# Performance work log

Measured on AMD Instinct MI355X. Metric: run time of the kernel, lower is better.

The kernel has to match this reference:

```python
import jax, jax.numpy as jnp
import numpy as np


def setup_inputs() -> dict:
    key = jax.random.key(0)
    k1, k2, k3 = jax.random.split(key, 3)
    B, C_in, H, W = 16, 256, 64, 64
    C_out, KH, KW = 256, 3, 3
    x = jax.random.normal(k1, (B, C_in, H, W), dtype=jnp.float32)
    # kaiming-uniform-like scale for realism
    fan_in = C_in * KH * KW
    bound = 1.0 / np.sqrt(fan_in)
    weights = jax.random.normal(k2, (C_out, C_in, KH, KW), dtype=jnp.float32) * bound
    bias = jax.random.uniform(k3, (C_out,), dtype=jnp.float32, minval=-bound, maxval=bound)
    return {"x": x, "weights": weights, "bias": bias}


def reference(x, weights, bias):
    # Conv2dApproximation with approximation_enable=False is an exact conv2d:
    # input is unfolded to [B, C*kh*kw, oh, ow], weights to [C_out, C*kh*kw],
    # and the MultiApp kernel performs the exact MAC (see exact matmul backward).
    # stride=(1,1), padding=(0,0), dilation=(1,1) per init_kwargs.
    out = jax.lax.conv_general_dilated(
        x, weights,
        window_strides=(1, 1),
        padding=((0, 0), (0, 0)),
        rhs_dilation=(1, 1),
        dimension_numbers=("NCHW", "OIHW", "NCHW"),
    )
    return out + bias[None, :, None, None]
```

## Files before the change

### kernel.cpp

```cpp
#include <hip/hip_runtime.h>
#include <stdint.h>

typedef short short8 __attribute__((ext_vector_type(8)));
typedef float f32x4 __attribute__((ext_vector_type(4)));

#define AS1 __attribute__((address_space(1)))
#define AS3 __attribute__((address_space(3)))

__device__ __forceinline__ void gl_lds16(const void* g, void* l) {
  __builtin_amdgcn_global_load_lds((const AS1 unsigned int*)g,
                                   (AS3 unsigned int*)l, 16, 0, 0);
}

__device__ __forceinline__ unsigned short f2bf(float f) {
  union { float f; unsigned int u; } v; v.f = f;
  return (unsigned short)((v.u + (((v.u >> 16) & 1u) + 0x7fffu)) >> 16);
}

__global__ __launch_bounds__(256) void xpose_kernel(const float* __restrict__ x,
                                                    unsigned short* __restrict__ xt) {
  __shared__ float tile[64][68];
  const int bid = blockIdx.x;
  const int cchunk = bid & 3;
  const int y = (bid >> 2) & 63;
  const int b = bid >> 8;
  const int t = threadIdx.x;
  const int ci0 = cchunk * 64;

  const int cc = t >> 2;
  const int xo = (t & 3) * 16;
  const float* src = x + (((size_t)(b * 256 + ci0 + cc) * 64 + y) * 64 + xo);
  float4 v0 = ((const float4*)src)[0];
  float4 v1 = ((const float4*)src)[1];
  float4 v2 = ((const float4*)src)[2];
  float4 v3 = ((const float4*)src)[3];
  *(float4*)&tile[cc][xo + 0]  = v0;
  *(float4*)&tile[cc][xo + 4]  = v1;
  *(float4*)&tile[cc][xo + 8]  = v2;
  *(float4*)&tile[cc][xo + 12] = v3;
  __syncthreads();

  const int xpos = t >> 2;
  const int ccg = (t & 3) * 16;
  unsigned int pk[8];
#pragma unroll
  for (int e = 0; e < 8; ++e) {
    unsigned int lo = f2bf(tile[ccg + 2 * e][xpos]);
    unsigned int hi = f2bf(tile[ccg + 2 * e + 1][xpos]);
    pk[e] = lo | (hi << 16);
  }
  unsigned short* dst = xt + ((size_t)(b * 4096 + y * 64 + xpos) * 256 + ci0 + ccg);
  uint4 w0; w0.x = pk[0]; w0.y = pk[1]; w0.z = pk[2]; w0.w = pk[3];
  uint4 w1; w1.x = pk[4]; w1.y = pk[5]; w1.z = pk[6]; w1.w = pk[7];
  ((uint4*)dst)[0] = w0;
  ((uint4*)dst)[1] = w1;
}

__global__ __launch_bounds__(256) void wpack_kernel(const float* __restrict__ w,
                                                    unsigned short* __restrict__ wrp) {
  const int idx = blockIdx.x * 256 + threadIdx.x;
  const int ci = idx & 255;
  const int co = (idx >> 8) & 255;
  const int p = idx >> 16;
  wrp[idx] = f2bf(w[(size_t)(co * 256 + ci) * 9 + p]);
}

__global__ __launch_bounds__(512, 2) void conv_mfma8(
    const unsigned short* __restrict__ xt,
    const unsigned short* __restrict__ wrp,
    const float* __restrict__ bias,
    float* __restrict__ out) {
  __shared__ unsigned short lds[4 * 16384];

  const int tid = threadIdx.x;
  const int lane = tid & 63;
  const int wv = tid >> 6;
  const int wr = wv >> 2;
  const int wc = wv & 3;
  const int bid = blockIdx.x;
  const int b = bid >> 4;
  const int oh0 = (bid & 15) * 4;

  const int srow = tid >> 2;
  const int sslot = tid & 3;
  const int sl = sslot ^ ((srow >> 1) & 3);
  const unsigned short* gA0 = wrp + (size_t)srow * 256 + sl * 8;
  const unsigned short* gA1 = wrp + (size_t)(128 + srow) * 256 + sl * 8;
  const unsigned short* gB[2];
#pragma unroll
  for (int i = 0; i < 2; ++i) {
    const int px = i * 128 + srow;
    const int prow = px >> 6, pcol = px & 63;
    const int y = min(oh0 + prow, 61);
    const int xc = min(pcol, 61);
    gB[i] = xt + ((size_t)(b * 64 + y) * 64 + xc) * 256 + sl * 8;
  }
  const unsigned ldsA0 = wv * 512;
  const unsigned ldsA1 = 4096 + wv * 512;
  const unsigned ldsB0 = 8192 + wv * 512;
  const unsigned ldsB1 = 12288 + wv * 512;

  int aoff[4], boff[8];
#pragma unroll
  for (int m = 0; m < 4; ++m) {
    const int row = wc * 64 + m * 16 + (lane & 15);
    const int s = (lane >> 4) ^ ((row >> 1) & 3);
    aoff[m] = row * 32 + s * 8;
  }
#pragma unroll
  for (int n = 0; n < 8; ++n) {
    const int row = wr * 128 + n * 16 + (lane & 15);
    const int s = (lane >> 4) ^ ((row >> 1) & 3);
    boff[n] = 8192 + row * 32 + s * 8;
  }

  auto stageA = [&](int kt) {
    const int tap = kt >> 3, chunk = (kt & 7) * 32;
    const int Aoff = tap * 65536 + chunk;
    unsigned short* base = lds + (kt & 3) * 16384;
    gl_lds16(gA0 + Aoff, base + ldsA0);
    gl_lds16(gA1 + Aoff, base + ldsA1);
  };
  auto stageB = [&](int kt) {
    const int tap = kt >> 3, chunk = (kt & 7) * 32;
    const int kh = (tap * 11) >> 5, kw = tap - kh * 3;
    const int Boff = (kh * 64 + kw) * 256 + chunk;
    unsigned short* base = lds + (kt & 3) * 16384;
    gl_lds16(gB[0] + Boff, base + ldsB0);
    gl_lds16(gB[1] + Boff, base + ldsB1);
  };

  f32x4 acc[4][8] = {};

  stageA(0); stageB(0);
  stageA(1); stageB(1);
  stageA(2); stageB(2);
  asm volatile("s_waitcnt vmcnt(8)" ::: "memory");
  __builtin_amdgcn_s_barrier();

  for (int kt = 0; kt < 72; ++kt) {
    unsigned short* buf = lds + (kt & 3) * 16384;
    short8 a[4], bq[4];
#pragma unroll
    for (int m = 0; m < 4; ++m) a[m] = *(const short8*)(buf + aoff[m]);
#pragma unroll
    for (int n = 0; n < 4; ++n) bq[n] = *(const short8*)(buf + boff[n]);
    if (kt < 69) stageA(kt + 3);
    __builtin_amdgcn_s_barrier();
    asm volatile("s_waitcnt lgkmcnt(0)" ::: "memory");
    __builtin_amdgcn_sched_barrier(0);
    __builtin_amdgcn_s_setprio(1);
#pragma unroll
    for (int m = 0; m < 4; ++m)
#pragma unroll
      for (int n = 0; n < 4; ++n)
        acc[m][n] = __builtin_amdgcn_mfma_f32_16x16x32_bf16(a[m], bq[n], acc[m][n], 0, 0, 0);
    __builtin_amdgcn_s_setprio(0);
    __builtin_amdgcn_s_barrier();
#pragma unroll
    for (int n = 0; n < 4; ++n) bq[n] = *(const short8*)(buf + boff[4 + n]);
    if (kt < 69) stageB(kt + 3);
    __builtin_amdgcn_s_barrier();
    asm volatile("s_waitcnt lgkmcnt(0)" ::: "memory");
    __builtin_amdgcn_sched_barrier(0);
    __builtin_amdgcn_s_setprio(1);
#pragma unroll
    for (int m = 0; m < 4; ++m)
#pragma unroll
      for (int n = 0; n < 4; ++n)
        acc[m][4 + n] = __builtin_amdgcn_mfma_f32_16x16x32_bf16(a[m], bq[n], acc[m][4 + n], 0, 0, 0);
    __builtin_amdgcn_s_setprio(0);
    if (kt <= 68)      asm volatile("s_waitcnt vmcnt(8)" ::: "memory");
    else if (kt == 69) asm volatile("s_waitcnt vmcnt(4)" ::: "memory");
    else if (kt == 70) asm volatile("s_waitcnt vmcnt(0)" ::: "memory");
    __builtin_amdgcn_s_barrier();
  }

  const int rb = (lane >> 4) * 4;
  const int colp = lane & 15;
  float bv[4][4];
#pragma unroll
  for (int m = 0; m < 4; ++m)
#pragma unroll
    for (int j = 0; j < 4; ++j)
      bv[m][j] = bias[wc * 64 + m * 16 + rb + j];
#pragma unroll
  for (int m = 0; m < 4; ++m) {
#pragma unroll
    for (int n = 0; n < 8; ++n) {
      const int px = wr * 128 + n * 16 + colp;
      const int prow = px >> 6, ow = px & 63;
      const int oh = oh0 + prow;
      if (ow < 62 && oh < 62) {
#pragma unroll
        for (int j = 0; j < 4; ++j) {
          const int co = wc * 64 + m * 16 + rb + j;
          out[((size_t)(b * 256 + co) * 62 + oh) * 62 + ow] = acc[m][n][j] + bv[m][j];
        }
      }
    }
  }
}

__global__ __launch_bounds__(256) void conv_naive(const float* __restrict__ x,
                                                  const float* __restrict__ wgt,
                                                  const float* __restrict__ bias,
                                                  float* __restrict__ out) {
  const size_t idx = (size_t)blockIdx.x * 256 + threadIdx.x;
  if (idx >= (size_t)16 * 256 * 62 * 62) return;
  const int ow = (int)(idx % 62);
  size_t r = idx / 62;
  const int oh = (int)(r % 62); r /= 62;
  const int co = (int)(r % 256);
  const int b = (int)(r / 256);
  float s = bias[co];
  for (int ci = 0; ci < 256; ++ci) {
    const float* xp = x + ((size_t)(b * 256 + ci) * 64 + oh) * 64 + ow;
    const float* wp = wgt + (size_t)(co * 256 + ci) * 9;
#pragma unroll
    for (int kh = 0; kh < 3; ++kh)
#pragma unroll
      for (int kw = 0; kw < 3; ++kw)
        s += xp[kh * 64 + kw] * wp[kh * 3 + kw];
  }
  out[idx] = s;
}

extern "C" void kernel_launch(void* const* d_in, const int* in_sizes, int n_in,
                              void* d_out, int out_size, void* d_ws, size_t ws_size,
                              hipStream_t stream) {
  const float* x = (const float*)d_in[0];
  const float* wgt = (const float*)d_in[1];
  const float* bias = (const float*)d_in[2];
  float* out = (float*)d_out;

  const size_t xt_elems = (size_t)16 * 64 * 64 * 256;
  const size_t wr_elems = (size_t)9 * 256 * 256;
  const size_t need = (xt_elems + wr_elems) * sizeof(unsigned short);

  if (ws_size < need) {
    conv_naive<<<61504, 256, 0, stream>>>(x, wgt, bias, out);
    return;
  }

  unsigned short* xt = (unsigned short*)d_ws;
  unsigned short* wrp = xt + xt_elems;

  xpose_kernel<<<4096, 256, 0, stream>>>(x, xt);
  wpack_kernel<<<2304, 256, 0, stream>>>(wgt, wrp);
  conv_mfma8<<<256, 512, 0, stream>>>(xt, wrp, bias, out);
}
```

Baseline: 101.2 us.

## Split output channels across blocks, shrink tiles and use 3-stage pipeline

```diff
diff --git a/kernel.cpp b/kernel.cpp
--- a/kernel.cpp
+++ b/kernel.cpp
@@ -65,42 +65,43 @@
   wrp[idx] = f2bf(w[(size_t)(co * 256 + ci) * 9 + p]);
 }
 
-__global__ __launch_bounds__(512, 2) void conv_mfma8(
+__global__ __launch_bounds__(512, 4) void conv_mfma2(
     const unsigned short* __restrict__ xt,
     const unsigned short* __restrict__ wrp,
     const float* __restrict__ bias,
     float* __restrict__ out) {
-  __shared__ unsigned short lds[4 * 16384];
+  __shared__ unsigned short lds[3 * 12288];
 
   const int tid = threadIdx.x;
   const int lane = tid & 63;
   const int wv = tid >> 6;
-  const int wr = wv >> 2;
-  const int wc = wv & 3;
+  const int wc = wv & 1;
+  const int wp = wv >> 1;
   const int bid = blockIdx.x;
-  const int b = bid >> 4;
+  const int cohalf = bid >> 8;
+  const int b = (bid >> 4) & 15;
   const int oh0 = (bid & 15) * 4;
-
-  const int srow = tid >> 2;
-  const int sslot = tid & 3;
-  const int sl = sslot ^ ((srow >> 1) & 3);
-  const unsigned short* gA0 = wrp + (size_t)srow * 256 + sl * 8;
-  const unsigned short* gA1 = wrp + (size_t)(128 + srow) * 256 + sl * 8;
+  const int co0 = cohalf * 128;
+
+  const int l2 = lane >> 2;
+  const int l3 = lane & 3;
+  const int rA = wv * 16 + l2;
+  const int slA = l3 ^ ((rA >> 1) & 3);
+  const unsigned short* gA = wrp + (size_t)(co0 + rA) * 256 + slA * 8;
   const unsigned short* gB[2];
 #pragma unroll
   for (int i = 0; i < 2; ++i) {
-    const int px = i * 128 + srow;
-    const int prow = px >> 6, pcol = px & 63;
-    const int y = min(oh0 + prow, 61);
-    const int xc = min(pcol, 61);
+    const int r = wv * 32 + i * 16 + l2;
+    const int sl = l3 ^ ((r >> 1) & 3);
+    const int y = min(oh0 + (r >> 6), 61);
+    const int xc = min(r & 63, 61);
     gB[i] = xt + ((size_t)(b * 64 + y) * 64 + xc) * 256 + sl * 8;
   }
-  const unsigned ldsA0 = wv * 512;
-  const unsigned ldsA1 = 4096 + wv * 512;
-  const unsigned ldsB0 = 8192 + wv * 512;
-  const unsigned ldsB1 = 12288 + wv * 512;
-
-  int aoff[4], boff[8];
+  const unsigned ldsA  = wv * 512;
+  const unsigned ldsB0 = 4096 + wv * 1024;
+  const unsigned ldsB1 = 4096 + wv * 1024 + 512;
+
+  int aoff[4], boff[4];
 #pragma unroll
   for (int m = 0; m < 4; ++m) {
     const int row = wc * 64 + m * 16 + (lane & 15);
@@ -108,45 +109,37 @@
     aoff[m] = row * 32 + s * 8;
   }
 #pragma unroll
-  for (int n = 0; n < 8; ++n) {
-    const int row = wr * 128 + n * 16 + (lane & 15);
+  for (int n = 0; n < 4; ++n) {
+    const int row = wp * 64 + n * 16 + (lane & 15);
     const int s = (lane >> 4) ^ ((row >> 1) & 3);
-    boff[n] = 8192 + row * 32 + s * 8;
-  }
-
-  auto stageA = [&](int kt) {
-    const int tap = kt >> 3, chunk = (kt & 7) * 32;
-    const int Aoff = tap * 65536 + chunk;
-    unsigned short* base = lds + (kt & 3) * 16384;
-    gl_lds16(gA0 + Aoff, base + ldsA0);
-    gl_lds16(gA1 + Aoff, base + ldsA1);
-  };
-  auto stageB = [&](int kt) {
+    boff[n] = 4096 + row * 32 + s * 8;
+  }
+
+  auto stage = [&](int kt) {
     const int tap = kt >> 3, chunk = (kt & 7) * 32;
     const int kh = (tap * 11) >> 5, kw = tap - kh * 3;
+    unsigned short* base = lds + (kt % 3) * 12288;
+    gl_lds16(gA + tap * 65536 + chunk, base + ldsA);
     const int Boff = (kh * 64 + kw) * 256 + chunk;
-    unsigned short* base = lds + (kt & 3) * 16384;
     gl_lds16(gB[0] + Boff, base + ldsB0);
     gl_lds16(gB[1] + Boff, base + ldsB1);
   };
 
-  f32x4 acc[4][8] = {};
-
-  stageA(0); stageB(0);
-  stageA(1); stageB(1);
-  stageA(2); stageB(2);
-  asm volatile("s_waitcnt vmcnt(8)" ::: "memory");
+  f32x4 acc[4][4] = {};
+
+  stage(0);
+  stage(1);
+  asm volatile("s_waitcnt vmcnt(3)" ::: "memory");
   __builtin_amdgcn_s_barrier();
 
   for (int kt = 0; kt < 72; ++kt) {
-    unsigned short* buf = lds + (kt & 3) * 16384;
-    short8 a[4], bq[4];
+    unsigned short* buf = lds + (kt % 3) * 12288;
+    short8 a[4], bb[4];
 #pragma unroll
     for (int m = 0; m < 4; ++m) a[m] = *(const short8*)(buf + aoff[m]);
 #pragma unroll
-    for (int n = 0; n < 4; ++n) bq[n] = *(const short8*)(buf + boff[n]);
-    if (kt < 69) stageA(kt + 3);
-    __builtin_amdgcn_s_barrier();
+    for (int n = 0; n < 4; ++n) bb[n] = *(const short8*)(buf + boff[n]);
+    if (kt < 70) stage(kt + 2);
     asm volatile("s_waitcnt lgkmcnt(0)" ::: "memory");
     __builtin_amdgcn_sched_barrier(0);
     __builtin_amdgcn_s_setprio(1);
@@ -154,49 +147,30 @@
     for (int m = 0; m < 4; ++m)
 #pragma unroll
       for (int n = 0; n < 4; ++n)
-        acc[m][n] = __builtin_amdgcn_mfma_f32_16x16x32_bf16(a[m], bq[n], acc[m][n], 0, 0, 0);
+        acc[m][n] = __builtin_amdgcn_mfma_f32_16x16x32_bf16(a[m], bb[n], acc[m][n], 0, 0, 0);
     __builtin_amdgcn_s_setprio(0);
-    __builtin_amdgcn_s_barrier();
-#pragma unroll
-    for (int n = 0; n < 4; ++n) bq[n] = *(const short8*)(buf + boff[4 + n]);
-    if (kt < 69) stageB(kt + 3);
-    __builtin_amdgcn_s_barrier();
-    asm volatile("s_waitcnt lgkmcnt(0)" ::: "memory");
-    __builtin_amdgcn_sched_barrier(0);
-    __builtin_amdgcn_s_setprio(1);
-#pragma unroll
-    for (int m = 0; m < 4; ++m)
-#pragma unroll
-      for (int n = 0; n < 4; ++n)
-        acc[m][4 + n] = __builtin_amdgcn_mfma_f32_16x16x32_bf16(a[m], bq[n], acc[m][4 + n], 0, 0, 0);
-    __builtin_amdgcn_s_setprio(0);
-    if (kt <= 68)      asm volatile("s_waitcnt vmcnt(8)" ::: "memory");
-    else if (kt == 69) asm volatile("s_waitcnt vmcnt(4)" ::: "memory");
+    if (kt < 70)       asm volatile("s_waitcnt vmcnt(3)" ::: "memory");
     else if (kt == 70) asm volatile("s_waitcnt vmcnt(0)" ::: "memory");
     __builtin_amdgcn_s_barrier();
   }
 
   const int rb = (lane >> 4) * 4;
   const int colp = lane & 15;
-  float bv[4][4];
-#pragma unroll
-  for (int m = 0; m < 4; ++m)
-#pragma unroll
-    for (int j = 0; j < 4; ++j)
-      bv[m][j] = bias[wc * 64 + m * 16 + rb + j];
 #pragma unroll
   for (int m = 0; m < 4; ++m) {
-#pragma unroll
-    for (int n = 0; n < 8; ++n) {
-      const int px = wr * 128 + n * 16 + colp;
+    const int co = co0 + wc * 64 + m * 16 + rb;
+    float bv[4];
+#pragma unroll
+    for (int j = 0; j < 4; ++j) bv[j] = bias[co + j];
+#pragma unroll
+    for (int n = 0; n < 4; ++n) {
+      const int px = wp * 64 + n * 16 + colp;
       const int prow = px >> 6, ow = px & 63;
       const int oh = oh0 + prow;
       if (ow < 62 && oh < 62) {
 #pragma unroll
-        for (int j = 0; j < 4; ++j) {
-          const int co = wc * 64 + m * 16 + rb + j;
-          out[((size_t)(b * 256 + co) * 62 + oh) * 62 + ow] = acc[m][n][j] + bv[m][j];
-        }
+        for (int j = 0; j < 4; ++j)
+          out[((size_t)(b * 256 + co + j) * 62 + oh) * 62 + ow] = acc[m][n][j] + bv[j];
       }
     }
   }
@@ -248,5 +222,5 @@
 
   xpose_kernel<<<4096, 256, 0, stream>>>(x, xt);
   wpack_kernel<<<2304, 256, 0, stream>>>(wgt, wrp);
-  conv_mfma8<<<256, 512, 0, stream>>>(xt, wrp, bias, out);
-}
+  conv_mfma2<<<512, 512, 0, stream>>>(xt, wrp, bias, out);
+}
```

Measured after the change: 107.2 us. +5.9%, slower.
